# Optimization experiments

Measured on AMD Instinct MI355X. Metric: run time of the kernel, lower is better.

## Reference

```python
import jax, jax.numpy as jnp
import numpy as np

B, S, D, H = 2, 2048, 1024, 16
MAX_DIST = 1024


def setup_inputs() -> dict:
    key = jax.random.key(0)
    ks = jax.random.split(key, 7)
    w = lambda k, shape: jax.random.normal(k, shape, jnp.float32) * 0.02
    return {
        "x": jax.random.normal(ks[0], (B, S, D), jnp.float32),
        "Wq": w(ks[1], (D, D)), "bq": jnp.zeros((D,), jnp.float32),
        "Wk": w(ks[2], (D, D)),
        "Wv": w(ks[3], (D, D)), "bv": jnp.zeros((D,), jnp.float32),
        "Wo": w(ks[4], (D, D)), "bo": jnp.zeros((D,), jnp.float32),
        "pos_bias": w(ks[5], (2 * MAX_DIST - 1, H)),
        "max_dist": MAX_DIST,
    }


def reference(x, Wq, bq, Wk, Wv, bv, Wo, bo, pos_bias, max_dist):
    b, s, d_model = x.shape
    h = pos_bias.shape[1]
    hd = d_model // h  # head dim
    scale = hd ** -0.25  # module's scale applied to (QK^T + rel_bias)

    split = lambda t: t.reshape(b, s, h, hd).transpose(0, 2, 1, 3)  # [b,h,s,hd]
    q = split(x @ Wq + bq)
    k = split(x @ Wk)          # key has no bias
    v = split(x @ Wv + bv)

    # raw QK^T (unscaled), as in the module
    scores = jnp.einsum('bhqd,bhkd->bhqk', q, k)

    # relative-position bias gather: clamp(i-j) -> table index
    pos = jnp.arange(s)[:, None] - jnp.arange(s)[None, :]
    pos = jnp.clip(pos, -max_dist + 1, max_dist - 1) + max_dist - 1
    rel_bias = pos_bias[pos].transpose(2, 0, 1)[None]  # [1,h,s,s]

    # SDPA with attn_mask = (scores + rel_bias)*scale adds it on top of QK^T/sqrt(hd)
    logits = scores * (1.0 / jnp.sqrt(jnp.float32(hd))) + (scores + rel_bias) * scale
    w = jax.nn.softmax(logits, axis=-1)

    out = jnp.einsum('bhqk,bhkd->bhqd', w, v)
    out = out.transpose(0, 2, 1, 3).reshape(b, s, d_model)
    return out @ Wo + bo
```

## Files before the change

kernel.cpp:

```cpp
#include <hip/hip_runtime.h>
#include <hip/hip_bf16.h>
#include <cstddef>
#include <cstdint>

#define BATCH   2
#define S_LEN   2048
#define D_MODEL 1024
#define NH      16
#define HD      64
#define MAXD    1024

#define SCORE_SCALE 0.47855339059327373f
#define BIAS_SCALE  0.35355339059327373f
#define FIXM 8.0f
#define LOG2E 1.4426950408889634f

typedef __attribute__((ext_vector_type(8))) short bf16x8;
typedef __attribute__((ext_vector_type(4))) short bf16x4;
typedef __attribute__((ext_vector_type(4))) float f32x4;

#if __has_builtin(__builtin_amdgcn_mfma_f32_16x16x16bf16_1k)
#define USE_1K 1
#else
#define USE_1K 0
#endif

static __device__ __forceinline__ unsigned short f2bf(float f) {
    __hip_bfloat16 h = __float2bfloat16(f);
    return *reinterpret_cast<unsigned short*>(&h);
}
static __device__ __forceinline__ float bf2f(unsigned short u) {
    union { unsigned int i; float f; } c;
    c.i = ((unsigned int)u) << 16;
    return c.f;
}

static __device__ __forceinline__ unsigned int pk_bf16(float lo, float hi) {
#if __has_builtin(__builtin_amdgcn_cvt_pk_bf16_f32)
    auto v = __builtin_amdgcn_cvt_pk_bf16_f32(lo, hi);
    unsigned int r;
    __builtin_memcpy(&r, &v, 4);
    return r;
#else
    __hip_bfloat162 h = __float22bfloat162_rn(make_float2(lo, hi));
    return *reinterpret_cast<unsigned int*>(&h);
#endif
}

#define GLDS(gp, lp) __builtin_amdgcn_global_load_lds( \
    (const __attribute__((address_space(1))) void*)(gp), \
    (__attribute__((address_space(3))) void*)(lp), 16, 0, 0)

__global__ __launch_bounds__(256) void prep(
    const float* __restrict__ x,
    const float* __restrict__ Wq, const float* __restrict__ Wk,
    const float* __restrict__ Wv, const float* __restrict__ Wo,
    const float* __restrict__ pos_bias,
    unsigned short* __restrict__ xb, unsigned short* __restrict__ Wqkvt,
    unsigned short* __restrict__ Wot,
    float* __restrict__ pb_t)
{
    __shared__ float t[32][33];
    const int bx = blockIdx.x, tid = threadIdx.x;

    if (bx < 2048) {
        const size_t i = ((size_t)bx * 256 + tid) * 8;
        const float4 a = *(const float4*)(x + i);
        const float4 b = *(const float4*)(x + i + 4);
        uint4 u;
        u.x = pk_bf16(a.x, a.y);
        u.y = pk_bf16(a.z, a.w);
        u.z = pk_bf16(b.x, b.y);
        u.w = pk_bf16(b.z, b.w);
        *(uint4*)(xb + i) = u;
    } else if (bx < 6144) {
        const int bx2 = bx - 2048;
        const int z = bx2 >> 10, inner = bx2 & 1023;
        const int gx = inner & 31, gy = inner >> 5;
        const float* W = (z == 0) ? Wq : (z == 1) ? Wk : (z == 2) ? Wv : Wo;
        unsigned short* hi = (z < 3) ? Wqkvt + (size_t)z * 1024 * 1024 : Wot;
        const int bxx = gx * 32, byy = gy * 32;
        const int tx = tid & 31, ty = tid >> 5;
        #pragma unroll
        for (int i = 0; i < 4; i++)
            t[ty + 8 * i][tx] = W[(size_t)(byy + ty + 8 * i) * 1024 + bxx + tx];
        __syncthreads();
        #pragma unroll
        for (int i = 0; i < 4; i++) {
            const float v = t[tx][ty + 8 * i];
            const size_t o = (size_t)(bxx + ty + 8 * i) * 1024 + byy + tx;
            hi[o] = f2bf(v);
        }
    } else {
        const int o0 = (bx - 6144) * 1024 + tid * 4;
        float v[4];
        #pragma unroll
        for (int j = 0; j < 4; j++) {
            const int o = o0 + j;
            const int hh = o >> 12, ii = o & 4095;
            int rel = ii - 2047;
            rel = min(max(rel, -(MAXD - 1)), MAXD - 1);
            v[j] = (BIAS_SCALE * pos_bias[(size_t)(rel + MAXD - 1) * NH + hh] - FIXM) * LOG2E;
        }
        *(float4*)&pb_t[o0] = *(const float4*)v;
    }
}

#define GBM 128
#define GBN 128
#define GBK 32

__global__ __launch_bounds__(256) void gemm_qkv(
    const unsigned short* __restrict__ A, const unsigned short* __restrict__ Bt,
    const float* __restrict__ bq, const float* __restrict__ bv,
    unsigned short* __restrict__ Cout)
{
    const int K = 1024;
    __shared__ __align__(16) unsigned short As[GBM][GBK];
    __shared__ __align__(16) unsigned short Bs[GBN][GBK];

    const int tid = threadIdx.x;
    const int wave = tid >> 6, lane = tid & 63;
    const int quad = lane >> 4, cl = lane & 15;
    const int wm = (wave & 1) * 64, wn = (wave >> 1) * 64;
    const int bm = blockIdx.y * GBM, bn = blockIdx.x * GBN;

    const int sr = wave * 32 + (lane >> 2);
    const int sc = (lane & 3) * 8;
    const unsigned short* aS0 = A  + (size_t)(bm + sr) * K + sc;
    const unsigned short* aS1 = aS0 + (size_t)16 * K;
    const unsigned short* bS0 = Bt + (size_t)(bn + sr) * K + sc;
    const unsigned short* bS1 = bS0 + (size_t)16 * K;
    unsigned short* aD0 = &As[wave * 32][0];
    unsigned short* aD1 = &As[wave * 32 + 16][0];
    unsigned short* bD0 = &Bs[wave * 32][0];
    unsigned short* bD1 = &Bs[wave * 32 + 16][0];

    f32x4 acc[4][4];
    #pragma unroll
    for (int mi = 0; mi < 4; mi++)
        #pragma unroll
        for (int ni = 0; ni < 4; ni++)
            #pragma unroll
            for (int r = 0; r < 4; r++) acc[mi][ni][r] = 0.f;

    for (int k0 = 0; k0 < K; k0 += GBK) {
        __syncthreads();
        GLDS(aS0, aD0); GLDS(aS1, aD1);
        GLDS(bS0, bD0); GLDS(bS1, bD1);
        aS0 += GBK; aS1 += GBK; bS0 += GBK; bS1 += GBK;
        __syncthreads();

        bf16x8 af[4], bf[4];
        #pragma unroll
        for (int mi = 0; mi < 4; mi++)
            af[mi] = *(const bf16x8*)&As[wm + mi * 16 + cl][quad * 8];
        #pragma unroll
        for (int ni = 0; ni < 4; ni++)
            bf[ni] = *(const bf16x8*)&Bs[wn + ni * 16 + cl][quad * 8];
        #pragma unroll
        for (int mi = 0; mi < 4; mi++)
            #pragma unroll
            for (int ni = 0; ni < 4; ni++)
                acc[mi][ni] = __builtin_amdgcn_mfma_f32_16x16x32_bf16(
                    af[mi], bf[ni], acc[mi][ni], 0, 0, 0);
    }

    #pragma unroll
    for (int ni = 0; ni < 4; ni++) {
        const int coln = bn + wn + ni * 16 + cl;
        const int region = coln >> 10, c = coln & 1023;
        const float bs = (region == 0) ? bq[c] : (region == 2) ? bv[c] : 0.f;
        #pragma unroll
        for (int mi = 0; mi < 4; mi++) {
            const int row0 = bm + wm + mi * 16 + quad * 4;
            if (region == 2) {
                const int hh = c >> 6, d = c & 63;
                const int bb = row0 >> 11, s0 = row0 & 2047;
                uint2 w;
                w.x = pk_bf16(acc[mi][ni][0] + bs, acc[mi][ni][1] + bs);
                w.y = pk_bf16(acc[mi][ni][2] + bs, acc[mi][ni][3] + bs);
                unsigned short* dst = Cout + (size_t)8 * 1024 * 1024
                    + (((size_t)bb * NH + hh) * HD + d) * S_LEN + s0;
                *(uint2*)dst = w;
            } else {
                unsigned short* dst = Cout + (size_t)region * 4 * 1024 * 1024;
                #pragma unroll
                for (int r = 0; r < 4; r++)
                    dst[(size_t)(row0 + r) * 1024 + c] = f2bf(acc[mi][ni][r] + bs);
            }
        }
    }
}

#define TQB 64
#define TKB 64

__global__ __launch_bounds__(256) void attn_mfma(
    const unsigned short* __restrict__ Q, const unsigned short* __restrict__ K,
    const unsigned short* __restrict__ VT, const float* __restrict__ pb_t,
    unsigned short* __restrict__ O)
{
    const int qt = blockIdx.x, h = blockIdx.y, b = blockIdx.z;
    const int tid  = threadIdx.x;
    const int wave = tid >> 6, lane = tid & 63;
    const int quad = lane >> 4, col = lane & 15;
    const int qbase = qt * TQB;
    const int qw = qbase + wave * 16;

    __shared__ __align__(16) unsigned short Ks[TKB][HD];
    __shared__ __align__(16) unsigned short Vs[HD][TKB];
#if !USE_1K
    __shared__ __align__(16) unsigned short Ps[4][16][TKB];
#endif

    bf16x8 qf[2];
    {
        const unsigned short* qp =
            &Q[((size_t)(b * S_LEN) + qw + col) * D_MODEL + h * HD + quad * 8];
        qf[0] = *(const bf16x8*)qp;
        qf[1] = *(const bf16x8*)(qp + 32);
    }

    f32x4 accO[4];
    #pragma unroll
    for (int nb = 0; nb < 4; nb++)
        #pragma unroll
        for (int r = 0; r < 4; r++) accO[nb][r] = 0.f;
#if USE_1K
    f32x4 accL;
    #pragma unroll
    for (int r = 0; r < 4; r++) accL[r] = 0.f;
    const bf16x4 vone = {(short)16256, (short)16256, (short)16256, (short)16256};
#else
    float lsum = 0.f;
#endif

    const int s0 = tid, s1 = 256 + tid;
    const int kr0 = s0 >> 3, kj0 = (s0 & 7) ^ (kr0 & 7);
    const int kr1 = s1 >> 3, kj1 = (s1 & 7) ^ (kr1 & 7);
    const unsigned short* kS0 = K + ((size_t)(b * S_LEN) + kr0) * D_MODEL + h * HD + kj0 * 8;
    const unsigned short* kS1 = K + ((size_t)(b * S_LEN) + kr1) * D_MODEL + h * HD + kj1 * 8;
    const size_t vbase = ((size_t)(b * NH + h) * HD) * S_LEN;
    const unsigned short* vS0 = VT + vbase + (size_t)kr0 * S_LEN + kj0 * 8;
    const unsigned short* vS1 = VT + vbase + (size_t)kr1 * S_LEN + kj1 * 8;
    unsigned short* kD = &Ks[0][0] + wave * 512;
    unsigned short* vD = &Vs[0][0] + wave * 512;

    const float* pbh = pb_t + h * 4096;
    const float* pb_lane = pbh + (qbase + wave * 16 + col - quad * 4 + 2047);
    const float SC2 = SCORE_SCALE * LOG2E;
    const int jsw = col & 7;

    for (int kb = 0; kb < S_LEN; kb += TKB) {
        __syncthreads();
        GLDS(kS0, kD); GLDS(kS1, kD + 2048);
        GLDS(vS0, vD); GLDS(vS1, vD + 2048);
        kS0 += (size_t)TKB * D_MODEL; kS1 += (size_t)TKB * D_MODEL;
        vS0 += TKB; vS1 += TKB;

        float bias_r[16];
        #pragma unroll
        for (int nb = 0; nb < 4; nb++)
            #pragma unroll
            for (int r = 0; r < 4; r++)
                bias_r[nb * 4 + r] = pb_lane[-(nb * 16 + r)];

        __syncthreads();

        f32x4 accS[4];
        #pragma unroll
        for (int nb = 0; nb < 4; nb++)
            #pragma unroll
            for (int r = 0; r < 4; r++) accS[nb][r] = 0.f;
        #pragma unroll
        for (int kk = 0; kk < 2; kk++)
            #pragma unroll
            for (int nb = 0; nb < 4; nb++) {
                const bf16x8 kf = *(const bf16x8*)
                    &Ks[nb * 16 + col][((kk * 4 + quad) ^ jsw) * 8];
                accS[nb] = __builtin_amdgcn_mfma_f32_16x16x32_bf16(kf, qf[kk], accS[nb], 0, 0, 0);
            }

#if USE_1K
        bf16x4 pf[4];
#endif
        #pragma unroll
        for (int nb = 0; nb < 4; nb++) {
            float pr[4];
            #pragma unroll
            for (int r = 0; r < 4; r++)
                pr[r] = __builtin_amdgcn_exp2f(fmaf(accS[nb][r], SC2, bias_r[nb * 4 + r]));
            uint2 w;
            w.x = pk_bf16(pr[0], pr[1]);
            w.y = pk_bf16(pr[2], pr[3]);
#if USE_1K
            union { uint2 u; bf16x4 v; } cv;
            cv.u = w;
            pf[nb] = cv.v;
            accL = __builtin_amdgcn_mfma_f32_16x16x16bf16_1k(vone, pf[nb], accL, 0, 0, 0);
#else
            #pragma unroll
            for (int r = 0; r < 4; r++) lsum += pr[r];
            const int jp = ((nb * 2 + (quad >> 1)) ^ jsw) * 8 + (quad & 1) * 4;
            *(uint2*)&Ps[wave][col][jp] = w;
#endif
        }

#if USE_1K
        #pragma unroll
        for (int s = 0; s < 4; s++) {
            #pragma unroll
            for (int nb = 0; nb < 4; nb++) {
                const bf16x4 vf = *(const bf16x4*)
                    &Vs[nb * 16 + col][(((2 * s + (quad >> 1)) ^ jsw) * 8) + (quad & 1) * 4];
                accO[nb] = __builtin_amdgcn_mfma_f32_16x16x16bf16_1k(vf, pf[s], accO[nb], 0, 0, 0);
            }
        }
#else
        #pragma unroll
        for (int kk = 0; kk < 2; kk++) {
            const bf16x8 af = *(const bf16x8*)
                &Ps[wave][col][((kk * 4 + quad) ^ jsw) * 8];
            #pragma unroll
            for (int nb = 0; nb < 4; nb++) {
                const bf16x8 vf = *(const bf16x8*)
                    &Vs[nb * 16 + col][((kk * 4 + quad) ^ jsw) * 8];
                accO[nb] = __builtin_amdgcn_mfma_f32_16x16x32_bf16(af, vf, accO[nb], 0, 0, 0);
            }
        }
#endif
        pb_lane -= TKB;
    }

#if USE_1K
    const float inv = 1.0f / accL[0];
    const size_t row = (size_t)(b * S_LEN) + qw + col;
    #pragma unroll
    for (int nb = 0; nb < 4; nb++) {
        uint2 w;
        w.x = pk_bf16(accO[nb][0] * inv, accO[nb][1] * inv);
        w.y = pk_bf16(accO[nb][2] * inv, accO[nb][3] * inv);
        *(uint2*)&O[row * D_MODEL + h * HD + nb * 16 + quad * 4] = w;
    }
#else
    lsum += __shfl_xor(lsum, 16);
    lsum += __shfl_xor(lsum, 32);
    #pragma unroll
    for (int r = 0; r < 4; r++) {
        const float inv = 1.0f / __shfl(lsum, quad * 4 + r);
        const size_t row = (size_t)(b * S_LEN) + qw + quad * 4 + r;
        #pragma unroll
        for (int nb = 0; nb < 4; nb++)
            O[row * D_MODEL + h * HD + nb * 16 + col] = f2bf(accO[nb][r] * inv);
    }
#endif
}

#define OBM 64
#define OBN 128

__global__ __launch_bounds__(256) void gemm_out(
    const unsigned short* __restrict__ A, const unsigned short* __restrict__ Bt,
    const float* __restrict__ bias, float* __restrict__ Cout)
{
    const int N = 1024, Kd = 1024;
    __shared__ __align__(16) unsigned short As[OBM][GBK];
    __shared__ __align__(16) unsigned short Bs[OBN][GBK];

    const int tid = threadIdx.x;
    const int wave = tid >> 6, lane = tid & 63;
    const int quad = lane >> 4, cl = lane & 15;
    const int wm = (wave & 1) * 32, wn = (wave >> 1) * 64;
    const int bm = blockIdx.y * OBM, bn = blockIdx.x * OBN;

    const int ar = tid >> 2, ac = (tid & 3) * 8;
    const unsigned short* aS = A + (size_t)(bm + ar) * Kd + ac;
    const unsigned short* hS0 = Bt + (size_t)(bn + ar) * Kd + ac;
    const unsigned short* hS1 = hS0 + (size_t)64 * Kd;
    unsigned short* aD  = &As[0][0] + wave * 512;
    unsigned short* hD0 = &Bs[0][0] + wave * 512;
    unsigned short* hD1 = hD0 + 2048;

    f32x4 acc[2][4];
    #pragma unroll
    for (int mi = 0; mi < 2; mi++)
        #pragma unroll
        for (int ni = 0; ni < 4; ni++)
            #pragma unroll
            for (int r = 0; r < 4; r++) acc[mi][ni][r] = 0.f;

    for (int k0 = 0; k0 < Kd; k0 += GBK) {
        __syncthreads();
        GLDS(aS, aD);
        GLDS(hS0, hD0); GLDS(hS1, hD1);
        aS += GBK; hS0 += GBK; hS1 += GBK;
        __syncthreads();

        bf16x8 af[2], bh[4];
        #pragma unroll
        for (int mi = 0; mi < 2; mi++)
            af[mi] = *(const bf16x8*)&As[wm + mi * 16 + cl][quad * 8];
        #pragma unroll
        for (int ni = 0; ni < 4; ni++)
            bh[ni] = *(const bf16x8*)&Bs[wn + ni * 16 + cl][quad * 8];
        #pragma unroll
        for (int mi = 0; mi < 2; mi++)
            #pragma unroll
            for (int ni = 0; ni < 4; ni++)
                acc[mi][ni] = __builtin_amdgcn_mfma_f32_16x16x32_bf16(
                    af[mi], bh[ni], acc[mi][ni], 0, 0, 0);
    }

    #pragma unroll
    for (int ni = 0; ni < 4; ni++) {
        const int coln = bn + wn + ni * 16 + cl;
        const float bs = bias[coln];
        #pragma unroll
        for (int mi = 0; mi < 2; mi++) {
            const int row0 = bm + wm + mi * 16 + quad * 4;
            #pragma unroll
            for (int r = 0; r < 4; r++)
                Cout[(size_t)(row0 + r) * N + coln] = acc[mi][ni][r] + bs;
        }
    }
}

extern "C" void kernel_launch(void* const* d_in, const int* in_sizes, int n_in,
                              void* d_out, int out_size, void* d_ws, size_t ws_size,
                              hipStream_t stream)
{
    const float* x        = (const float*)d_in[0];
    const float* Wq       = (const float*)d_in[1];
    const float* bq       = (const float*)d_in[2];
    const float* Wk       = (const float*)d_in[3];
    const float* Wv       = (const float*)d_in[4];
    const float* bv       = (const float*)d_in[5];
    const float* Wo       = (const float*)d_in[6];
    const float* bo       = (const float*)d_in[7];
    const float* pos_bias = (const float*)d_in[8];
    float* out = (float*)d_out;

    const size_t ELEMS  = (size_t)BATCH * S_LEN * D_MODEL;
    const size_t WELEMS = (size_t)D_MODEL * D_MODEL;
    unsigned short* xb     = (unsigned short*)d_ws;
    unsigned short* Wqkvt  = xb + ELEMS;
    unsigned short* Wot    = Wqkvt + 3 * WELEMS;
    unsigned short* QKV    = Wot + WELEMS;
    unsigned short* Qb     = QKV;
    unsigned short* Kb     = Qb + ELEMS;
    unsigned short* VTb    = Kb + ELEMS;
    unsigned short* Ab     = VTb + ELEMS;
    float* pb_t            = (float*)(Ab + ELEMS);

    prep<<<6208, 256, 0, stream>>>(x, Wq, Wk, Wv, Wo, pos_bias,
                                   xb, Wqkvt, Wot, pb_t);

    gemm_qkv<<<dim3(3072 / GBN, 4096 / GBM), 256, 0, stream>>>(
        xb, Wqkvt, bq, bv, QKV);

    attn_mfma<<<dim3(S_LEN / TQB, NH, BATCH), 256, 0, stream>>>(
        Qb, Kb, VTb, pb_t, Ab);

    gemm_out<<<dim3(1024 / OBN, 4096 / OBM), 256, 0, stream>>>(
        Ab, Wot, bo, out);
}
```

Before: 224.3 us.

## Fuse all four stages into one cooperative persistent kernel with grid syncs

Turns prep, QKV GEMM, attention and output GEMM into device functions that share one LDS arena, and runs them inside a single cooperative kernel of 1024 blocks, separated by grid.sync(). The aim is to remove the launch gaps and tail idle time between the four kernels. In exchange, every stage is forced onto a fixed 1024-block grid: some stages leave blocks idle, and the shared arena plus occupancy hint may limit scheduling. If the cooperative launch fails, it falls back to separate kernels.

```diff
diff --git a/kernel.cpp b/kernel.cpp
--- a/kernel.cpp
+++ b/kernel.cpp
@@ -1,7 +1,10 @@
 #include <hip/hip_runtime.h>
 #include <hip/hip_bf16.h>
+#include <hip/hip_cooperative_groups.h>
 #include <cstddef>
 #include <cstdint>
+
+namespace cg = cooperative_groups;
 
 #define BATCH   2
 #define S_LEN   2048
@@ -21,18 +24,15 @@
 
 #if __has_builtin(__builtin_amdgcn_mfma_f32_16x16x16bf16_1k)
 #define USE_1K 1
+#define ARENA_BYTES 16384
 #else
 #define USE_1K 0
+#define ARENA_BYTES 24576
 #endif
 
 static __device__ __forceinline__ unsigned short f2bf(float f) {
     __hip_bfloat16 h = __float2bfloat16(f);
     return *reinterpret_cast<unsigned short*>(&h);
-}
-static __device__ __forceinline__ float bf2f(unsigned short u) {
-    union { unsigned int i; float f; } c;
-    c.i = ((unsigned int)u) << 16;
-    return c.f;
 }
 
 static __device__ __forceinline__ unsigned int pk_bf16(float lo, float hi) {
@@ -51,17 +51,16 @@
     (const __attribute__((address_space(1))) void*)(gp), \
     (__attribute__((address_space(3))) void*)(lp), 16, 0, 0)
 
-__global__ __launch_bounds__(256) void prep(
+static __device__ __forceinline__ void prep_body(
+    int bx, int tid, unsigned char* smem,
     const float* __restrict__ x,
     const float* __restrict__ Wq, const float* __restrict__ Wk,
     const float* __restrict__ Wv, const float* __restrict__ Wo,
     const float* __restrict__ pos_bias,
     unsigned short* __restrict__ xb, unsigned short* __restrict__ Wqkvt,
-    unsigned short* __restrict__ Wot,
-    float* __restrict__ pb_t)
-{
-    __shared__ float t[32][33];
-    const int bx = blockIdx.x, tid = threadIdx.x;
+    unsigned short* __restrict__ Wot, float* __restrict__ pb_t)
+{
+    float (*t)[33] = (float(*)[33])smem;
 
     if (bx < 2048) {
         const size_t i = ((size_t)bx * 256 + tid) * 8;
@@ -91,6 +90,7 @@
             const size_t o = (size_t)(bxx + ty + 8 * i) * 1024 + byy + tx;
             hi[o] = f2bf(v);
         }
+        __syncthreads();
     } else {
         const int o0 = (bx - 6144) * 1024 + tid * 4;
         float v[4];
@@ -106,24 +106,22 @@
     }
 }
 
-#define GBM 128
-#define GBN 128
 #define GBK 32
 
-__global__ __launch_bounds__(256) void gemm_qkv(
+static __device__ __forceinline__ void qkv_body(
+    int bnIdx, int bmIdx, int tid, unsigned char* smem,
     const unsigned short* __restrict__ A, const unsigned short* __restrict__ Bt,
     const float* __restrict__ bq, const float* __restrict__ bv,
     unsigned short* __restrict__ Cout)
 {
     const int K = 1024;
-    __shared__ __align__(16) unsigned short As[GBM][GBK];
-    __shared__ __align__(16) unsigned short Bs[GBN][GBK];
-
-    const int tid = threadIdx.x;
+    unsigned short (*As)[GBK] = (unsigned short(*)[GBK])smem;
+    unsigned short (*Bs)[GBK] = (unsigned short(*)[GBK])(smem + 8192);
+
     const int wave = tid >> 6, lane = tid & 63;
     const int quad = lane >> 4, cl = lane & 15;
     const int wm = (wave & 1) * 64, wn = (wave >> 1) * 64;
-    const int bm = blockIdx.y * GBM, bn = blockIdx.x * GBN;
+    const int bm = bmIdx * 128, bn = bnIdx * 128;
 
     const int sr = wave * 32 + (lane >> 2);
     const int sc = (lane & 3) * 8;
@@ -165,6 +163,7 @@
                 acc[mi][ni] = __builtin_amdgcn_mfma_f32_16x16x32_bf16(
                     af[mi], bf[ni], acc[mi][ni], 0, 0, 0);
     }
+    __syncthreads();
 
     #pragma unroll
     for (int ni = 0; ni < 4; ni++) {
@@ -196,22 +195,21 @@
 #define TQB 64
 #define TKB 64
 
-__global__ __launch_bounds__(256) void attn_mfma(
+static __device__ __forceinline__ void attn_body(
+    int qt, int h, int b, int tid, unsigned char* smem,
     const unsigned short* __restrict__ Q, const unsigned short* __restrict__ K,
     const unsigned short* __restrict__ VT, const float* __restrict__ pb_t,
     unsigned short* __restrict__ O)
 {
-    const int qt = blockIdx.x, h = blockIdx.y, b = blockIdx.z;
-    const int tid  = threadIdx.x;
     const int wave = tid >> 6, lane = tid & 63;
     const int quad = lane >> 4, col = lane & 15;
     const int qbase = qt * TQB;
     const int qw = qbase + wave * 16;
 
-    __shared__ __align__(16) unsigned short Ks[TKB][HD];
-    __shared__ __align__(16) unsigned short Vs[HD][TKB];
+    unsigned short (*Ks)[HD]  = (unsigned short(*)[HD])smem;
+    unsigned short (*Vs)[TKB] = (unsigned short(*)[TKB])(smem + 8192);
 #if !USE_1K
-    __shared__ __align__(16) unsigned short Ps[4][16][TKB];
+    unsigned short (*Ps)[TKB] = (unsigned short(*)[TKB])(smem + 16384);
 #endif
 
     bf16x8 qf[2];
@@ -301,9 +299,11 @@
             accL = __builtin_amdgcn_mfma_f32_16x16x16bf16_1k(vone, pf[nb], accL, 0, 0, 0);
 #else
             #pragma unroll
-            for (int r = 0; r < 4; r++) lsum += pr[r];
+            for (int r = 0; r < 4; r++) {
+                lsum += pr[r];
+            }
             const int jp = ((nb * 2 + (quad >> 1)) ^ jsw) * 8 + (quad & 1) * 4;
-            *(uint2*)&Ps[wave][col][jp] = w;
+            *(uint2*)&Ps[wave * 16 + col][jp] = w;
 #endif
         }
 
@@ -321,7 +321,7 @@
         #pragma unroll
         for (int kk = 0; kk < 2; kk++) {
             const bf16x8 af = *(const bf16x8*)
-                &Ps[wave][col][((kk * 4 + quad) ^ jsw) * 8];
+                &Ps[wave * 16 + col][((kk * 4 + quad) ^ jsw) * 8];
             #pragma unroll
             for (int nb = 0; nb < 4; nb++) {
                 const bf16x8 vf = *(const bf16x8*)
@@ -332,6 +332,7 @@
 #endif
         pb_lane -= TKB;
     }
+    __syncthreads();
 
 #if USE_1K
     const float inv = 1.0f / accL[0];
@@ -357,22 +358,19 @@
 #endif
 }
 
-#define OBM 64
-#define OBN 128
-
-__global__ __launch_bounds__(256) void gemm_out(
+static __device__ __forceinline__ void out_body(
+    int bnIdx, int bmIdx, int tid, unsigned char* smem,
     const unsigned short* __restrict__ A, const unsigned short* __restrict__ Bt,
     const float* __restrict__ bias, float* __restrict__ Cout)
 {
     const int N = 1024, Kd = 1024;
-    __shared__ __align__(16) unsigned short As[OBM][GBK];
-    __shared__ __align__(16) unsigned short Bs[OBN][GBK];
-
-    const int tid = threadIdx.x;
+    unsigned short (*As)[GBK] = (unsigned short(*)[GBK])smem;
+    unsigned short (*Bs)[GBK] = (unsigned short(*)[GBK])(smem + 4096);
+
     const int wave = tid >> 6, lane = tid & 63;
     const int quad = lane >> 4, cl = lane & 15;
     const int wm = (wave & 1) * 32, wn = (wave >> 1) * 64;
-    const int bm = blockIdx.y * OBM, bn = blockIdx.x * OBN;
+    const int bm = bmIdx * 64, bn = bnIdx * 128;
 
     const int ar = tid >> 2, ac = (tid & 3) * 8;
     const unsigned short* aS = A + (size_t)(bm + ar) * Kd + ac;
@@ -424,6 +422,73 @@
                 Cout[(size_t)(row0 + r) * N + coln] = acc[mi][ni][r] + bs;
         }
     }
+}
+
+__global__ __launch_bounds__(256, 4) void fused_all(
+    const float* x, const float* Wq, const float* Wk, const float* Wv,
+    const float* Wo, const float* pos_bias, const float* bq, const float* bv,
+    const float* bo, unsigned short* xb, unsigned short* Wqkvt,
+    unsigned short* Wot, unsigned short* QKV, unsigned short* Ab,
+    float* pb_t, float* out)
+{
+    cg::grid_group grid = cg::this_grid();
+    __shared__ __align__(16) unsigned char smem[ARENA_BYTES];
+    const int tid = threadIdx.x;
+    const int nb = gridDim.x;
+
+    for (int vb = blockIdx.x; vb < 6208; vb += nb)
+        prep_body(vb, tid, smem, x, Wq, Wk, Wv, Wo, pos_bias, xb, Wqkvt, Wot, pb_t);
+    grid.sync();
+
+    if ((int)blockIdx.x < 768)
+        qkv_body(blockIdx.x % 24, blockIdx.x / 24, tid, smem, xb, Wqkvt, bq, bv, QKV);
+    grid.sync();
+
+    {
+        const int vb = blockIdx.x;
+        attn_body(vb & 31, (vb >> 5) & 15, vb >> 9, tid, smem,
+                  QKV, QKV + (size_t)4 * 1024 * 1024,
+                  QKV + (size_t)8 * 1024 * 1024, pb_t, Ab);
+    }
+    grid.sync();
+
+    if ((int)blockIdx.x < 512)
+        out_body(blockIdx.x % 8, blockIdx.x / 8, tid, smem, Ab, Wot, bo, out);
+}
+
+__global__ __launch_bounds__(256) void prep_k(
+    const float* x, const float* Wq, const float* Wk, const float* Wv,
+    const float* Wo, const float* pos_bias, unsigned short* xb,
+    unsigned short* Wqkvt, unsigned short* Wot, float* pb_t)
+{
+    __shared__ __align__(16) unsigned char smem[4224];
+    prep_body(blockIdx.x, threadIdx.x, smem, x, Wq, Wk, Wv, Wo, pos_bias,
+              xb, Wqkvt, Wot, pb_t);
+}
+
+__global__ __launch_bounds__(256) void qkv_k(
+    const unsigned short* A, const unsigned short* Bt,
+    const float* bq, const float* bv, unsigned short* Cout)
+{
+    __shared__ __align__(16) unsigned char smem[16384];
+    qkv_body(blockIdx.x, blockIdx.y, threadIdx.x, smem, A, Bt, bq, bv, Cout);
+}
+
+__global__ __launch_bounds__(256) void attn_k(
+    const unsigned short* Q, const unsigned short* K,
+    const unsigned short* VT, const float* pb_t, unsigned short* O)
+{
+    __shared__ __align__(16) unsigned char smem[ARENA_BYTES];
+    attn_body(blockIdx.x, blockIdx.y, blockIdx.z, threadIdx.x, smem,
+              Q, K, VT, pb_t, O);
+}
+
+__global__ __launch_bounds__(256) void out_k(
+    const unsigned short* A, const unsigned short* Bt,
+    const float* bias, float* Cout)
+{
+    __shared__ __align__(16) unsigned char smem[12288];
+    out_body(blockIdx.x, blockIdx.y, threadIdx.x, smem, A, Bt, bias, Cout);
 }
 
 extern "C" void kernel_launch(void* const* d_in, const int* in_sizes, int n_in,
@@ -447,21 +512,24 @@
     unsigned short* Wqkvt  = xb + ELEMS;
     unsigned short* Wot    = Wqkvt + 3 * WELEMS;
     unsigned short* QKV    = Wot + WELEMS;
-    unsigned short* Qb     = QKV;
-    unsigned short* Kb     = Qb + ELEMS;
-    unsigned short* VTb    = Kb + ELEMS;
-    unsigned short* Ab     = VTb + ELEMS;
+    unsigned short* Ab     = QKV + 3 * ELEMS;
     float* pb_t            = (float*)(Ab + ELEMS);
 
-    prep<<<6208, 256, 0, stream>>>(x, Wq, Wk, Wv, Wo, pos_bias,
-                                   xb, Wqkvt, Wot, pb_t);
-
-    gemm_qkv<<<dim3(3072 / GBN, 4096 / GBM), 256, 0, stream>>>(
-        xb, Wqkvt, bq, bv, QKV);
-
-    attn_mfma<<<dim3(S_LEN / TQB, NH, BATCH), 256, 0, stream>>>(
-        Qb, Kb, VTb, pb_t, Ab);
-
-    gemm_out<<<dim3(1024 / OBN, 4096 / OBM), 256, 0, stream>>>(
-        Ab, Wot, bo, out);
-}
+    void* args[] = {
+        (void*)&x, (void*)&Wq, (void*)&Wk, (void*)&Wv, (void*)&Wo,
+        (void*)&pos_bias, (void*)&bq, (void*)&bv, (void*)&bo,
+        (void*)&xb, (void*)&Wqkvt, (void*)&Wot, (void*)&QKV, (void*)&Ab,
+        (void*)&pb_t, (void*)&out,
+    };
+    hipError_t err = hipLaunchCooperativeKernel(
+        (const void*)fused_all, dim3(1024), dim3(256), args, 0, stream);
+
+    if (err != hipSuccess) {
+        prep_k<<<6208, 256, 0, stream>>>(x, Wq, Wk, Wv, Wo, pos_bias,
+                                         xb, Wqkvt, Wot, pb_t);
+        qkv_k<<<dim3(24, 32), 256, 0, stream>>>(xb, Wqkvt, bq, bv, QKV);
+        attn_k<<<dim3(32, 16, 2), 256, 0, stream>>>(
+            QKV, QKV + 4 * ELEMS / 4, QKV + 2 * ELEMS, pb_t, Ab);
+        out_k<<<dim3(8, 64), 256, 0, stream>>>(Ab, Wot, bo, out);
+    }
+}
```

Result: slower. 617.1 us (+175.1%).
